# Performance work log

Measured on AMD Instinct MI355X. Metric: run time of the kernel, lower is better.

## Reference

```python
import jax, jax.numpy as jnp
import numpy as np

LEAKY_SLOPE = 0.2
LN_EPS = 1e-5
SOFTMAX_EPS = 1e-16  # PyG softmax denominator eps


def setup_inputs() -> dict:
    key = jax.random.key(0)
    ks = jax.random.split(key, 8)
    N, E, F, H, C, ED = 100000, 1600000, 64, 8, 8, 16
    s = 1.0 / np.sqrt(F)
    return {
        "x": jax.random.normal(ks[0], (N, F), jnp.float32),
        "edge_index": jax.random.randint(ks[1], (2, E), 0, N, jnp.int32),
        "edge_attr": jax.random.normal(ks[2], (E, ED), jnp.float32),
        "W_l": jax.random.normal(ks[3], (H * C, F), jnp.float32) * s,
        "b_l": jnp.zeros((H * C,), jnp.float32),
        "W_r": jax.random.normal(ks[4], (H * C, F), jnp.float32) * s,
        "b_r": jnp.zeros((H * C,), jnp.float32),
        "W_e": jax.random.normal(ks[5], (H * C, ED), jnp.float32) * (1.0 / np.sqrt(ED)),
        "att": jax.random.normal(ks[6], (1, H, C), jnp.float32) * (1.0 / np.sqrt(C)),
        "bias": jnp.zeros((H * C,), jnp.float32),
        "gamma": jnp.ones((F,), jnp.float32),
        "beta": jnp.zeros((F,), jnp.float32),
    }


def reference(x, edge_index, edge_attr, W_l, b_l, W_r, b_r, W_e, att, bias, gamma, beta):
    N, F = x.shape
    H, C = att.shape[1], att.shape[2]
    src, dst = edge_index[0], edge_index[1]  # PyG: row0=source(j), row1=target(i)

    xl = (x @ W_l.T + b_l).reshape(N, H, C)   # lin_l -> x_j side
    xr = (x @ W_r.T + b_r).reshape(N, H, C)   # lin_r -> x_i side
    e = (edge_attr @ W_e.T).reshape(-1, H, C)  # lin_edge (no bias)

    m = jax.nn.leaky_relu(xl[src] + xr[dst] + e, LEAKY_SLOPE)  # [E,H,C]
    logits = jnp.einsum('ehc,hc->eh', m, att[0])               # [E,H]

    # per-destination segment softmax
    mx = jax.ops.segment_max(logits, dst, num_segments=N)      # [N,H]
    mx = jnp.where(jnp.isfinite(mx), mx, 0.0)                  # nodes w/o in-edges
    ex = jnp.exp(logits - mx[dst])
    denom = jax.ops.segment_sum(ex, dst, num_segments=N)
    alpha = ex / (denom[dst] + SOFTMAX_EPS)                    # [E,H]; dropout is identity in eval

    agg = jax.ops.segment_sum(alpha[:, :, None] * xl[src], dst, num_segments=N)  # [N,H,C]
    out = agg.reshape(N, H * C) + bias

    h = out + x  # residual
    mu = jnp.mean(h, axis=-1, keepdims=True)
    var = jnp.mean((h - mu) ** 2, axis=-1, keepdims=True)
    hn = (h - mu) * jax.lax.rsqrt(var + LN_EPS) * gamma + beta
    return jax.nn.relu(hn)
```

## Files before the change

kernel.cpp:

```cpp
#include <hip/hip_runtime.h>

#define LEAKY 0.2f
#define LN_EPS 1e-5f
#define SM_EPS 1e-16f
#define CAP 64
#define WPAD 68

#define BIN_SHIFT 8
#define MAXBINS   448
#define CHUNK_A   5632
#define BCAP      4608
#define EMASK     0x1FFFFF
#define NPW       4

__global__ __launch_bounds__(256) void k_node_linear(
    const float* __restrict__ x,
    const float* __restrict__ Wl,
    const float* __restrict__ bl,
    const float* __restrict__ Wr,
    const float* __restrict__ br,
    float* __restrict__ xl, float* __restrict__ xr, int N)
{
    __shared__ __align__(16) float sW[64 * WPAD];

    const int tid = threadIdx.x;
    const int side = blockIdx.x & 1;
    const float* __restrict__ W  = side ? Wr : Wl;
    const float* __restrict__ bv = side ? br : bl;
    float* __restrict__ dst      = side ? xr : xl;

    for (int i = tid; i < 4096; i += 256)
        sW[(i >> 6) * WPAD + (i & 63)] = W[i];
    __syncthreads();

    const int lane = tid & 63;
    float4 wq[16];
    #pragma unroll
    for (int q = 0; q < 16; ++q)
        wq[q] = *(const float4*)&sW[lane * WPAD + q * 4];
    const float bb = bv[lane];

    const int stream0 = (blockIdx.x >> 1) * 4 + (tid >> 6);
    const int nstream = (gridDim.x >> 1) * 4;
    for (int n = stream0; n < N; n += nstream) {
        const float4* xrow = (const float4*)(x + (long long)n * 64);
        float a = bb;
        #pragma unroll
        for (int q = 0; q < 16; ++q) {
            const float4 xv = xrow[q];
            const float4 w  = wq[q];
            a = fmaf(xv.x, w.x, fmaf(xv.y, w.y, fmaf(xv.z, w.z, fmaf(xv.w, w.w, a))));
        }
        dst[(long long)n * 64 + lane] = a;
    }
}

__global__ __launch_bounds__(256) void k_bucket(
    const int* __restrict__ ei, int* __restrict__ deg,
    int2* __restrict__ slot2, int E)
{
    const int e = blockIdx.x * 256 + threadIdx.x;
    if (e >= E) return;
    const int dst = ei[E + e];
    const int pos = atomicAdd(deg + dst, 1);
    if (pos < CAP) slot2[(long long)dst * CAP + pos] = make_int2(e, ei[e]);
}

__global__ __launch_bounds__(256) void k_binA(
    const int* __restrict__ ei,
    int* __restrict__ binCnt,
    int2* __restrict__ binArr,
    int E, int nbins)
{
    __shared__ int2 ord[CHUNK_A];
    __shared__ unsigned short ordBin[CHUNK_A];
    __shared__ int cnt[MAXBINS], offs[MAXBINS], cur[MAXBINS], resB[MAXBINS];

    const int tid  = threadIdx.x;
    const int lane = tid & 63;
    const int ebase = blockIdx.x * CHUNK_A;
    const int nE = (E - ebase < CHUNK_A) ? (E - ebase) : CHUNK_A;
    const int* __restrict__ dstp = ei + E + ebase;
    const int* __restrict__ srcp = ei + ebase;

    for (int b = tid; b < MAXBINS; b += 256) { cnt[b] = 0; cur[b] = 0; }
    __syncthreads();

    for (int i = tid; i < nE; i += 256)
        atomicAdd(&cnt[dstp[i] >> BIN_SHIFT], 1);
    __syncthreads();

    if (tid < 64) {
        int carry = 0;
        #pragma unroll
        for (int seg = 0; seg < MAXBINS / 64; ++seg) {
            const int v = cnt[seg * 64 + lane];
            int s = v;
            #pragma unroll
            for (int off = 1; off < 64; off <<= 1) {
                const int t = __shfl_up(s, off, 64);
                if (lane >= off) s += t;
            }
            offs[seg * 64 + lane] = carry + s - v;
            carry += __shfl(s, 63, 64);
        }
    }
    __syncthreads();

    for (int i = tid; i < nE; i += 256) {
        const int d = dstp[i];
        const int b = d >> BIN_SHIFT;
        const int pos = atomicAdd(&cur[b], 1);
        const int at = offs[b] + pos;
        ord[at] = make_int2((ebase + i) | ((d & ((1 << BIN_SHIFT) - 1)) << 21), srcp[i]);
        ordBin[at] = (unsigned short)b;
    }
    __syncthreads();

    for (int b = tid; b < nbins; b += 256) {
        const int c = cnt[b];
        resB[b] = c ? atomicAdd(&binCnt[b], c) : 0;
    }
    __syncthreads();

    for (int i = tid; i < nE; i += 256) {
        const int b = ordBin[i];
        const int k = resB[b] + (i - offs[b]);
        if (k < BCAP) binArr[(long long)b * BCAP + k] = ord[i];
    }
}

__global__ __launch_bounds__(256) void k_binB(
    const int* __restrict__ binCnt,
    const int2* __restrict__ binArr,
    int* __restrict__ deg,
    int2* __restrict__ slot2,
    int N)
{
    __shared__ int2 ord2[BCAP];
    __shared__ int cnt2[256], offs2[256], cur2[256];

    const int b = blockIdx.x;
    const int tid  = threadIdx.x;
    const int lane = tid & 63;
    const int dst0 = b << BIN_SHIFT;
    int nb = binCnt[b];
    if (nb > BCAP) nb = BCAP;
    const int2* __restrict__ src = binArr + (long long)b * BCAP;

    cnt2[tid] = 0; cur2[tid] = 0;
    __syncthreads();

    for (int i = tid; i < nb; i += 256)
        atomicAdd(&cnt2[((unsigned)src[i].x >> 21) & 0xFF], 1);
    __syncthreads();

    if (tid < 64) {
        int carry = 0;
        #pragma unroll
        for (int seg = 0; seg < 4; ++seg) {
            const int v = cnt2[seg * 64 + lane];
            int s = v;
            #pragma unroll
            for (int off = 1; off < 64; off <<= 1) {
                const int t = __shfl_up(s, off, 64);
                if (lane >= off) s += t;
            }
            offs2[seg * 64 + lane] = carry + s - v;
            carry += __shfl(s, 63, 64);
        }
    }
    __syncthreads();

    for (int i = tid; i < nb; i += 256) {
        const int2 p = src[i];
        const int d = ((unsigned)p.x >> 21) & 0xFF;
        const int pos = atomicAdd(&cur2[d], 1);
        ord2[offs2[d] + pos] = make_int2(p.x & EMASK, p.y);
    }
    __syncthreads();

    const int nd = (N - dst0 < 256) ? (N - dst0) : 256;
    if (tid < nd) deg[dst0 + tid] = cnt2[tid];

    const int wv = tid >> 6;
    for (int d = wv; d < nd; d += 4) {
        int c = cnt2[d];
        if (c > CAP) c = CAP;
        if (lane < c) slot2[(long long)(dst0 + d) * CAP + lane] = ord2[offs2[d] + lane];
    }
}

__global__ __launch_bounds__(256) void k_gather(
    const float* __restrict__ ea,
    const float* __restrict__ We,
    const float* __restrict__ att,
    const float* __restrict__ xl, const float* __restrict__ xr,
    const int* __restrict__ deg, const int2* __restrict__ slot2,
    const float* __restrict__ x,
    const float* __restrict__ bias, const float* __restrict__ gamma,
    const float* __restrict__ beta,
    float* __restrict__ out, int N)
{
    const int lane = threadIdx.x & 63;
    const int wid  = blockIdx.x * 4 + (threadIdx.x >> 6);
    const int n0   = wid * NPW;
    if (n0 >= N) return;

    const float4* w4 = (const float4*)(We + lane * 16);
    const float4 w0 = w4[0], w1 = w4[1], w2 = w4[2], w3 = w4[3];
    const float attv  = att[lane];
    const float biasv = bias[lane];
    const float gv    = gamma[lane];
    const float bev   = beta[lane];

    for (int j = 0; j < NPW; ++j) {
        const int n = n0 + j;
        if (n >= N) break;

        const float xrv = xr[(long long)n * 64 + lane];
        const int d = min(deg[n], CAP);

        int veid = 0, vsrc = 0;
        if (lane < d) {
            const int2 es = slot2[(long long)n * CAP + lane];
            veid = es.x;
            vsrc = es.y;
        }

        float acc = 0.f;
        float ns  = 0.f;

        float xlA = 0.f, xlB = 0.f;
        float4 a0, a1, a2, a3, b0, b1, b2, b3;
        a0 = a1 = a2 = a3 = b0 = b1 = b2 = b3 = make_float4(0.f, 0.f, 0.f, 0.f);

#define FETCH(jj, XLV, E0, E1, E2, E3) do {                      \
        const int s_ = __shfl(vsrc, (jj), 64);                   \
        const int e_ = __shfl(veid, (jj), 64);                   \
        XLV = xl[(long long)s_ * 64 + lane];                     \
        const float4* p_ = (const float4*)(ea + (long long)e_ * 16); \
        E0 = p_[0]; E1 = p_[1]; E2 = p_[2]; E3 = p_[3];          \
    } while (0)

#define COMPUTE(XLV, E0, E1, E2, E3) do {                        \
        float ep = E0.x*w0.x + E0.y*w0.y + E0.z*w0.z + E0.w*w0.w \
                 + E1.x*w1.x + E1.y*w1.y + E1.z*w1.z + E1.w*w1.w \
                 + E2.x*w2.x + E2.y*w2.y + E2.z*w2.z + E2.w*w2.w \
                 + E3.x*w3.x + E3.y*w3.y + E3.z*w3.z + E3.w*w3.w;\
        float m = XLV + xrv + ep;                                \
        m = (m > 0.f) ? m : LEAKY * m;           \
        float p = m * attv;                                      \
        p += __shfl_xor(p, 1, 64);                               \
        p += __shfl_xor(p, 2, 64);                               \
        p += __shfl_xor(p, 4, 64);                               \
        const float ex = __expf(p);                              \
        ns  += ex;                                               \
        acc = fmaf(ex, XLV, acc);                                \
    } while (0)

        if (d > 0) FETCH(0, xlA, a0, a1, a2, a3);
        if (d > 1) FETCH(1, xlB, b0, b1, b2, b3);

        for (int i = 0; i < d; i += 2) {
            COMPUTE(xlA, a0, a1, a2, a3);
            if (i + 2 < d) FETCH(i + 2, xlA, a0, a1, a2, a3);
            if (i + 1 < d) {
                COMPUTE(xlB, b0, b1, b2, b3);
                if (i + 3 < d) FETCH(i + 3, xlB, b0, b1, b2, b3);
            }
        }
#undef FETCH
#undef COMPUTE

        const float a = acc / (ns + SM_EPS);
        const float hv = a + biasv + x[(long long)n * 64 + lane];

        float s = hv;
        #pragma unroll
        for (int off = 32; off; off >>= 1) s += __shfl_xor(s, off, 64);
        const float mu = s * (1.f / 64.f);
        const float dd = hv - mu;
        float v = dd * dd;
        #pragma unroll
        for (int off = 32; off; off >>= 1) v += __shfl_xor(v, off, 64);
        const float var = v * (1.f / 64.f);

        float hn = dd * rsqrtf(var + LN_EPS) * gv + bev;
        out[(long long)n * 64 + lane] = (hn > 0.f) ? hn : 0.f;
    }
}

extern "C" void kernel_launch(void* const* d_in, const int* in_sizes, int n_in,
                              void* d_out, int out_size, void* d_ws, size_t ws_size,
                              hipStream_t stream) {
    (void)n_in; (void)out_size;

    const float* x     = (const float*)d_in[0];
    const int*   ei    = (const int*)d_in[1];
    const float* ea    = (const float*)d_in[2];
    const float* Wl    = (const float*)d_in[3];
    const float* bl    = (const float*)d_in[4];
    const float* Wr    = (const float*)d_in[5];
    const float* br    = (const float*)d_in[6];
    const float* We    = (const float*)d_in[7];
    const float* att   = (const float*)d_in[8];
    const float* bias  = (const float*)d_in[9];
    const float* gamma = (const float*)d_in[10];
    const float* beta  = (const float*)d_in[11];

    const int N = in_sizes[0] / 64;
    const int E = in_sizes[1] / 2;
    const int nbins = (N + (1 << BIN_SHIFT) - 1) >> BIN_SHIFT;

    float* w = (float*)d_ws;
    float* xl   = w;                      w += (size_t)N * 64;
    float* xr   = w;                      w += (size_t)N * 64;
    int* deg    = (int*)w;
    int* binCnt = deg + N;
    int2* slot2 = (int2*)(binCnt + MAXBINS);
    int2* binArr = slot2 + (size_t)N * CAP;
    const size_t needed = ((char*)(binArr + (size_t)nbins * BCAP)) - (char*)d_ws;

    float* out = (float*)d_out;

    const bool binned = (nbins <= MAXBINS) && (E <= (1 << 21)) &&
                        (ws_size >= needed);

    hipMemsetAsync(deg, 0, ((size_t)N + MAXBINS) * sizeof(int), stream);

    k_node_linear<<<2048, 256, 0, stream>>>(x, Wl, bl, Wr, br, xl, xr, N);

    if (binned) {
        const int nbA = (E + CHUNK_A - 1) / CHUNK_A;
        k_binA<<<nbA, 256, 0, stream>>>(ei, binCnt, binArr, E, nbins);
        k_binB<<<nbins, 256, 0, stream>>>(binCnt, binArr, deg, slot2, N);
    } else {
        k_bucket<<<(E + 255) / 256, 256, 0, stream>>>(ei, deg, slot2, E);
    }

    k_gather<<<(N + 16 * 1 - 1) / 16, 256, 0, stream>>>(
        ea, We, att, xl, xr, deg, slot2, x, bias, gamma, beta, out, N);
}
```

Before: 620.8 us.

## Fuse node linear with binning pass and deepen gather prefetch to four edges

```diff
diff --git a/kernel.cpp b/kernel.cpp
--- a/kernel.cpp
+++ b/kernel.cpp
@@ -12,18 +12,89 @@
 #define BCAP      4608
 #define EMASK     0x1FFFFF
 #define NPW       4
-
-__global__ __launch_bounds__(256) void k_node_linear(
+#define NL_BLOCKS 2048
+
+#define PREP_LDS 63488
+
+__global__ __launch_bounds__(256) void k_prepA(
     const float* __restrict__ x,
     const float* __restrict__ Wl,
     const float* __restrict__ bl,
     const float* __restrict__ Wr,
     const float* __restrict__ br,
-    float* __restrict__ xl, float* __restrict__ xr, int N)
+    float* __restrict__ xl, float* __restrict__ xr,
+    const int* __restrict__ ei,
+    int* __restrict__ binCnt,
+    int2* __restrict__ binArr,
+    int N, int E, int nbins)
 {
-    __shared__ __align__(16) float sW[64 * WPAD];
-
-    const int tid = threadIdx.x;
+    extern __shared__ __align__(16) char smem[];
+    const int tid  = threadIdx.x;
+    const int lane = tid & 63;
+
+    if (blockIdx.x >= NL_BLOCKS) {
+        int2* ord = (int2*)smem;
+        int*  cnt = (int*)(smem + 45056);
+        int*  offs = (int*)(smem + 46848);
+        int*  cur = (int*)(smem + 48640);
+        int*  resB = (int*)(smem + 50432);
+        unsigned short* ordBin = (unsigned short*)(smem + 52224);
+
+        const int ebase = (blockIdx.x - NL_BLOCKS) * CHUNK_A;
+        const int nE = (E - ebase < CHUNK_A) ? (E - ebase) : CHUNK_A;
+        const int* __restrict__ dstp = ei + E + ebase;
+        const int* __restrict__ srcp = ei + ebase;
+
+        for (int b = tid; b < MAXBINS; b += 256) { cnt[b] = 0; cur[b] = 0; }
+        __syncthreads();
+
+        for (int i = tid; i < nE; i += 256)
+            atomicAdd(&cnt[dstp[i] >> BIN_SHIFT], 1);
+        __syncthreads();
+
+        if (tid < 64) {
+            int carry = 0;
+            #pragma unroll
+            for (int seg = 0; seg < MAXBINS / 64; ++seg) {
+                const int v = cnt[seg * 64 + lane];
+                int s = v;
+                #pragma unroll
+                for (int off = 1; off < 64; off <<= 1) {
+                    const int t = __shfl_up(s, off, 64);
+                    if (lane >= off) s += t;
+                }
+                offs[seg * 64 + lane] = carry + s - v;
+                carry += __shfl(s, 63, 64);
+            }
+        }
+        __syncthreads();
+
+        for (int i = tid; i < nE; i += 256) {
+            const int d = dstp[i];
+            const int b = d >> BIN_SHIFT;
+            const int pos = atomicAdd(&cur[b], 1);
+            const int at = offs[b] + pos;
+            ord[at] = make_int2((ebase + i) | ((d & ((1 << BIN_SHIFT) - 1)) << 21), srcp[i]);
+            ordBin[at] = (unsigned short)b;
+        }
+        __syncthreads();
+
+        for (int b = tid; b < nbins; b += 256) {
+            const int c = cnt[b];
+            resB[b] = c ? atomicAdd(&binCnt[b], c) : 0;
+        }
+        __syncthreads();
+
+        for (int i = tid; i < nE; i += 256) {
+            const int b = ordBin[i];
+            const int k = resB[b] + (i - offs[b]);
+            if (k < BCAP) binArr[(long long)b * BCAP + k] = ord[i];
+        }
+        return;
+    }
+
+    float* sW = (float*)smem;
+
     const int side = blockIdx.x & 1;
     const float* __restrict__ W  = side ? Wr : Wl;
     const float* __restrict__ bv = side ? br : bl;
@@ -33,7 +104,6 @@
         sW[(i >> 6) * WPAD + (i & 63)] = W[i];
     __syncthreads();
 
-    const int lane = tid & 63;
     float4 wq[16];
     #pragma unroll
     for (int q = 0; q < 16; ++q)
@@ -41,7 +111,7 @@
     const float bb = bv[lane];
 
     const int stream0 = (blockIdx.x >> 1) * 4 + (tid >> 6);
-    const int nstream = (gridDim.x >> 1) * 4;
+    const int nstream = (NL_BLOCKS >> 1) * 4;
     for (int n = stream0; n < N; n += nstream) {
         const float4* xrow = (const float4*)(x + (long long)n * 64);
         float a = bb;
@@ -64,70 +134,6 @@
     const int dst = ei[E + e];
     const int pos = atomicAdd(deg + dst, 1);
     if (pos < CAP) slot2[(long long)dst * CAP + pos] = make_int2(e, ei[e]);
-}
-
-__global__ __launch_bounds__(256) void k_binA(
-    const int* __restrict__ ei,
-    int* __restrict__ binCnt,
-    int2* __restrict__ binArr,
-    int E, int nbins)
-{
-    __shared__ int2 ord[CHUNK_A];
-    __shared__ unsigned short ordBin[CHUNK_A];
-    __shared__ int cnt[MAXBINS], offs[MAXBINS], cur[MAXBINS], resB[MAXBINS];
-
-    const int tid  = threadIdx.x;
-    const int lane = tid & 63;
-    const int ebase = blockIdx.x * CHUNK_A;
-    const int nE = (E - ebase < CHUNK_A) ? (E - ebase) : CHUNK_A;
-    const int* __restrict__ dstp = ei + E + ebase;
-    const int* __restrict__ srcp = ei + ebase;
-
-    for (int b = tid; b < MAXBINS; b += 256) { cnt[b] = 0; cur[b] = 0; }
-    __syncthreads();
-
-    for (int i = tid; i < nE; i += 256)
-        atomicAdd(&cnt[dstp[i] >> BIN_SHIFT], 1);
-    __syncthreads();
-
-    if (tid < 64) {
-        int carry = 0;
-        #pragma unroll
-        for (int seg = 0; seg < MAXBINS / 64; ++seg) {
-            const int v = cnt[seg * 64 + lane];
-            int s = v;
-            #pragma unroll
-            for (int off = 1; off < 64; off <<= 1) {
-                const int t = __shfl_up(s, off, 64);
-                if (lane >= off) s += t;
-            }
-            offs[seg * 64 + lane] = carry + s - v;
-            carry += __shfl(s, 63, 64);
-        }
-    }
-    __syncthreads();
-
-    for (int i = tid; i < nE; i += 256) {
-        const int d = dstp[i];
-        const int b = d >> BIN_SHIFT;
-        const int pos = atomicAdd(&cur[b], 1);
-        const int at = offs[b] + pos;
-        ord[at] = make_int2((ebase + i) | ((d & ((1 << BIN_SHIFT) - 1)) << 21), srcp[i]);
-        ordBin[at] = (unsigned short)b;
-    }
-    __syncthreads();
-
-    for (int b = tid; b < nbins; b += 256) {
-        const int c = cnt[b];
-        resB[b] = c ? atomicAdd(&binCnt[b], c) : 0;
-    }
-    __syncthreads();
-
-    for (int i = tid; i < nE; i += 256) {
-        const int b = ordBin[i];
-        const int k = resB[b] + (i - offs[b]);
-        if (k < BCAP) binArr[(long long)b * BCAP + k] = ord[i];
-    }
 }
 
 __global__ __launch_bounds__(256) void k_binB(
@@ -231,9 +237,11 @@
         float acc = 0.f;
         float ns  = 0.f;
 
-        float xlA = 0.f, xlB = 0.f;
+        float xlA = 0.f, xlB = 0.f, xlC = 0.f, xlD = 0.f;
         float4 a0, a1, a2, a3, b0, b1, b2, b3;
+        float4 c0, c1, c2, c3, d0, d1, d2, d3;
         a0 = a1 = a2 = a3 = b0 = b1 = b2 = b3 = make_float4(0.f, 0.f, 0.f, 0.f);
+        c0 = c1 = c2 = c3 = d0 = d1 = d2 = d3 = make_float4(0.f, 0.f, 0.f, 0.f);
 
 #define FETCH(jj, XLV, E0, E1, E2, E3) do {                      \
         const int s_ = __shfl(vsrc, (jj), 64);                   \
@@ -261,13 +269,23 @@
 
         if (d > 0) FETCH(0, xlA, a0, a1, a2, a3);
         if (d > 1) FETCH(1, xlB, b0, b1, b2, b3);
-
-        for (int i = 0; i < d; i += 2) {
+        if (d > 2) FETCH(2, xlC, c0, c1, c2, c3);
+        if (d > 3) FETCH(3, xlD, d0, d1, d2, d3);
+
+        for (int i = 0; i < d; i += 4) {
             COMPUTE(xlA, a0, a1, a2, a3);
-            if (i + 2 < d) FETCH(i + 2, xlA, a0, a1, a2, a3);
+            if (i + 4 < d) FETCH(i + 4, xlA, a0, a1, a2, a3);
             if (i + 1 < d) {
                 COMPUTE(xlB, b0, b1, b2, b3);
-                if (i + 3 < d) FETCH(i + 3, xlB, b0, b1, b2, b3);
+                if (i + 5 < d) FETCH(i + 5, xlB, b0, b1, b2, b3);
+                if (i + 2 < d) {
+                    COMPUTE(xlC, c0, c1, c2, c3);
+                    if (i + 6 < d) FETCH(i + 6, xlC, c0, c1, c2, c3);
+                    if (i + 3 < d) {
+                        COMPUTE(xlD, d0, d1, d2, d3);
+                        if (i + 7 < d) FETCH(i + 7, xlD, d0, d1, d2, d3);
+                    }
+                }
             }
         }
 #undef FETCH
@@ -329,16 +347,17 @@
 
     hipMemsetAsync(deg, 0, ((size_t)N + MAXBINS) * sizeof(int), stream);
 
-    k_node_linear<<<2048, 256, 0, stream>>>(x, Wl, bl, Wr, br, xl, xr, N);
-
     if (binned) {
         const int nbA = (E + CHUNK_A - 1) / CHUNK_A;
-        k_binA<<<nbA, 256, 0, stream>>>(ei, binCnt, binArr, E, nbins);
+        k_prepA<<<NL_BLOCKS + nbA, 256, PREP_LDS, stream>>>(
+            x, Wl, bl, Wr, br, xl, xr, ei, binCnt, binArr, N, E, nbins);
         k_binB<<<nbins, 256, 0, stream>>>(binCnt, binArr, deg, slot2, N);
     } else {
+        k_prepA<<<NL_BLOCKS, 256, PREP_LDS, stream>>>(
+            x, Wl, bl, Wr, br, xl, xr, ei, binCnt, binArr, N, E, nbins);
         k_bucket<<<(E + 255) / 256, 256, 0, stream>>>(ei, deg, slot2, E);
     }
 
-    k_gather<<<(N + 16 * 1 - 1) / 16, 256, 0, stream>>>(
+    k_gather<<<(N + 15) / 16, 256, 0, stream>>>(
         ea, We, att, xl, xr, deg, slot2, x, bias, gamma, beta, out, N);
 }
```

New measurement: 628.9 us. Within noise of the previous version (+1.3%).
